# Optimization experiments

Measured on AMD Instinct MI355X. Metric: run time of the kernel, lower is better.

## Reference

```python
import jax, jax.numpy as jnp
import numpy as np

N = 4096          # residues (2 chains x 2048)
CHAINS = 2
LMAX = 2
L = (LMAX + 1) ** 2            # 9 spherical coefficients
BBC = 32                       # bb_channels
NBB = 3                        # n_bb_atoms - 1
SPH = BBC + NBB                # 35 sphere channels fed to attention
KNN = 20
LRK = 40
HEADS = 8
HC = 32
VC = HC // 4                   # attn_value_channels = 8
EDGE_F = 32                    # 16 RBF + 16 positional
L_IDX = np.repeat(np.arange(LMAX + 1), 2 * np.arange(LMAX + 1) + 1)  # degree of each of the 9 coeffs


def so3_linear(x, w, b):
    # x: [N,L,Cin]; w: [LMAX+1,Cin,Cout] shared across m within each degree l; bias only on l=0
    out = jnp.einsum('nlc,lcd->nld', x, w[L_IDX])
    return out.at[:, 0, :].add(b)


def _rbf(d):
    mu = jnp.linspace(0.0, 20.0, 16)
    sigma = 20.0 / 16
    return jnp.exp(-(((d[..., None] - mu) / sigma) ** 2))


def _edge_pos_embed(src, dst):
    d = (src - dst).astype(jnp.float32)
    freq = jnp.exp(jnp.arange(0, 16, 2, dtype=jnp.float32) * (-np.log(10000.0) / 16))
    ang = d[:, None] * freq
    return jnp.concatenate([jnp.cos(ang), jnp.sin(ang)], axis=-1)


def setup_inputs():
    key = jax.random.key(0)
    ks = jax.random.split(key, 16)
    n = lambda i, shp, s=1.0: jax.random.normal(ks[i], shp) * s
    return {
        'X_ca': n(0, (N, 3), 10.0),
        'bb_rel': n(1, (N, NBB, 3)),
        'bb_features': n(2, (N, L, BBC)),
        'batch': jnp.repeat(jnp.arange(CHAINS), N // CHAINS),
        'x_mask': jax.random.uniform(ks[3], (N,)) < 0.02,
        'noising_mask': jax.random.uniform(ks[4], (N,)) < 0.5,
        'attn_w1': n(5, (2 * SPH + EDGE_F, HC), 0.05), 'attn_b1': jnp.zeros((HC,)),
        'attn_w2': n(6, (HC, HEADS), 0.05), 'attn_b2': jnp.zeros((HEADS,)),
        'wv': n(7, (LMAX + 1, SPH, HEADS * VC), 0.05), 'bv': jnp.zeros((HEADS * VC,)),
        'wo': n(8, (LMAX + 1, HEADS * VC, BBC), 0.05), 'bo': jnp.zeros((BBC,)),
        'wg': n(9, (BBC, BBC), 0.05), 'bg': jnp.zeros((BBC,)),
        'wf': n(10, (LMAX + 1, BBC, BBC), 0.05), 'bf': jnp.zeros((BBC,)),
        'w_xca': n(11, (LMAX + 1, BBC, 1), 0.05), 'b_xca': jnp.zeros((1,)),
        'w_gate': n(12, (BBC, 1), 0.05), 'b_gate': jnp.zeros((1,)),
        'w_bb': n(13, (LMAX + 1, BBC, NBB), 0.05), 'b_bb': jnp.zeros((NBB,)),
    }


def reference(X_ca, bb_rel, bb_features, batch, x_mask, noising_mask,
              attn_w1, attn_b1, attn_w2, attn_b2, wv, bv, wo, bo, wg, bg, wf, bf,
              w_xca, b_xca, w_gate, b_gate, w_bb, b_bb):
    Nn = X_ca.shape[0]
    BIG = jnp.float32(1e30)
    # ---- graph construction (knn_graph + sample_inv_cubic_edges) ----
    x2 = jnp.sum(X_ca * X_ca, axis=-1)
    D2 = jnp.maximum(x2[:, None] + x2[None, :] - 2.0 * (X_ca @ X_ca.T), 0.0)  # [N,N]
    same = batch[:, None] == batch[None, :]
    eye = jnp.eye(Nn, dtype=bool)
    mask_pair = x_mask[:, None] | x_mask[None, :]
    invalid = (~same) | eye | mask_pair
    knn_idx = jax.lax.top_k(-jnp.where(invalid, BIG, D2), KNN)[1]   # [N,KNN] sources per target
    # long-range: inverse-cubic distance weights, Gumbel top-k sampling, excluding knn picks
    logits = jnp.where(invalid, -BIG, -1.5 * jnp.log(D2 + 1e-6))
    rows = jnp.arange(Nn)[:, None]
    logits = logits.at[rows, knn_idx].set(-BIG)
    gumb = jax.random.gumbel(jax.random.key(1), (Nn, Nn))
    lr_idx = jax.lax.top_k(logits + gumb, LRK)[1]                   # [N,LRK]
    src = jnp.concatenate([knn_idx.reshape(-1), lr_idx.reshape(-1)])
    dst = jnp.concatenate([jnp.repeat(jnp.arange(Nn), KNN), jnp.repeat(jnp.arange(Nn), LRK)])
    # ---- edge features: RBF(dist) + relative positional embedding ----
    dvec = X_ca[src] - X_ca[dst]
    dist = jnp.linalg.norm(dvec, axis=-1)
    edge_feat = jnp.concatenate([_rbf(dist), _edge_pos_embed(src, dst)], axis=-1)  # [M,32]
    # ---- assemble SO3 node embedding [N,L,35] ----
    node = jnp.zeros((Nn, L, SPH), X_ca.dtype)
    node = node.at[:, :, :BBC].set(bb_features)
    node = node.at[:, 1:4, BBC:].set(jnp.swapaxes(bb_rel, -1, -2))  # l=1 coeffs carry bb_rel
    node = node.at[:, 0, SPH - 1].set(noising_mask.astype(X_ca.dtype))
    # ---- equivariant graph attention (simplified TransBlockV2) ----
    inv = node[:, 0, :]                                             # invariant (l=0) features
    a_in = jnp.concatenate([inv[src], inv[dst], edge_feat], axis=-1)
    h = jax.nn.silu(a_in @ attn_w1 + attn_b1)
    logit = h @ attn_w2 + attn_b2                                   # [M,HEADS]
    mx = jax.ops.segment_max(logit, dst, num_segments=Nn)
    p = jnp.exp(logit - mx[dst])
    Z = jax.ops.segment_sum(p, dst, num_segments=Nn)
    alpha = p / (Z[dst] + 1e-9)                                     # segment softmax per target/head
    v = so3_linear(node, wv, bv)[src].reshape(-1, L, HEADS, VC)     # gather source values
    msg = (v * alpha[:, None, :, None]).reshape(-1, L, HEADS * VC)
    agg = jax.ops.segment_sum(msg, dst, num_segments=Nn)            # scatter to targets
    out = so3_linear(agg, wo, bo)                                   # [N,L,32]
    gate = jax.nn.silu(out[:, 0, :] @ wg + bg)                      # invariant-gated FFN
    out = out + so3_linear(out, wf, bf) * gate[:, None, :]
    # ---- coordinate / backbone updates ----
    upd_x = so3_linear(out, w_xca, b_xca)                           # [N,L,1]
    vec = upd_x[:, 1:4, 0]                                          # l=1 -> 3-vector
    g2 = jax.nn.softplus(out[:, 0, :] @ w_gate + b_gate)            # [N,1]
    new_X = X_ca + jnp.where(noising_mask[:, None], vec * g2, 0.0)
    upd_bb = so3_linear(out, w_bb, b_bb)                            # [N,L,3]
    dbb = jnp.swapaxes(upd_bb[:, 1:4, :], -1, -2)                   # [N,3,3]
    new_bb = bb_rel + jnp.where(noising_mask[:, None, None], dbb, 0.0)
    return new_X, new_bb, out
```

## Files before the change

kernel.cpp:

```cpp
#include <hip/hip_runtime.h>
#include <hip/hip_bf16.h>
#include <stdint.h>

#define NN 4096
#define CS 2048
#define KNN 20
#define LRK 40
#define EPN 60
#define NE (NN*EPN)
#define SPHC 35
#define BBCC 32
#define NHEAD 8
#define HVD 64
#define HCD 32
#define LT 9
#define MAXC 384

#define INVAL_D2 0xFFFFFFFEu
#define CONSUMED 0xFFFFFFFFu

__device__ __forceinline__ float bf2f(__hip_bfloat16 x) { return __bfloat162float(x); }

__device__ __forceinline__ float fast_exp(float x) {
  return __builtin_amdgcn_exp2f(x * 1.4426950408889634f);
}
__device__ __forceinline__ float fast_cos(float a) {
  float rev = a * 0.15915494309189535f;
  rev = rev - __builtin_rintf(rev);
  return __builtin_amdgcn_cosf(rev);
}
__device__ __forceinline__ float fast_sin(float a) {
  float rev = a * 0.15915494309189535f;
  rev = rev - __builtin_rintf(rev);
  return __builtin_amdgcn_sinf(rev);
}

__device__ __forceinline__ float neglogu_f(int i, int j) {
  uint32_t c = ((uint32_t)(i & 2047) << 12) | (uint32_t)j;
  const uint32_t ks0 = 0u, ks1 = 1u, ks2 = 0x1BD11BDBu;
  uint32_t x0 = c + ks0;
  uint32_t x1 = (c + 0x800000u) + ks1;
#define TF_R(r) { x0 += x1; x1 = (x1 << (r)) | (x1 >> (32 - (r))); x1 ^= x0; }
  TF_R(13) TF_R(15) TF_R(26) TF_R(6)   x0 += ks1; x1 += ks2 + 1u;
  TF_R(17) TF_R(29) TF_R(16) TF_R(24)  x0 += ks2; x1 += ks0 + 2u;
  TF_R(13) TF_R(15) TF_R(26) TF_R(6)   x0 += ks0; x1 += ks1 + 3u;
  TF_R(17) TF_R(29) TF_R(16) TF_R(24)  x0 += ks1; x1 += ks2 + 4u;
  TF_R(13) TF_R(15) TF_R(26) TF_R(6)   x0 += ks2; x1 += ks0 + 5u;
#undef TF_R
  uint32_t b = (i >= 2048) ? x1 : x0;
  float u = __uint_as_float((b >> 9) | 0x3F800000u) - 1.0f;
  u = u + 1.17549435e-38f;
  return -logf(u);
}

__global__ void prep_kernel(const float* __restrict__ X,
                            const int* __restrict__ batch,
                            const int* __restrict__ xmask,
                            float4* __restrict__ Xw, uint32_t* __restrict__ bm) {
#pragma clang fp contract(off)
  int n = blockIdx.x * blockDim.x + threadIdx.x;
  if (n >= NN) return;
  float x = X[n*3+0], y = X[n*3+1], z = X[n*3+2];
  float x2 = (x*x + y*y) + z*z;
  Xw[n] = make_float4(x, y, z, x2);
  bm[n] = ((uint32_t)batch[n] << 1) | (xmask[n] ? 1u : 0u);
}

__global__ __launch_bounds__(256) void nodeproj_kernel(const float* __restrict__ bbf,
                                                       const int* __restrict__ nmask,
                                                       const float* __restrict__ w1,
                                                       const float* __restrict__ b1,
                                                       float* __restrict__ Pn,
                                                       float* __restrict__ Pd) {
  int tid = threadIdx.x;
  int t = tid & 31;
  int n = blockIdx.x * 8 + (tid >> 5);
  float bv_ = bbf[(size_t)n * (LT*BBCC) + t];
  float an = 0.f, ad = b1[t];
  #pragma unroll 8
  for (int c = 0; c < BBCC; c++) {
    float bc = __shfl(bv_, (tid & 32) + c, 64);
    an = fmaf(bc, w1[c * HCD + t], an);
    ad = fmaf(bc, w1[(SPHC + c) * HCD + t], ad);
  }
  float nm = nmask[n] ? 1.f : 0.f;
  an = fmaf(nm, w1[34 * HCD + t], an);
  ad = fmaf(nm, w1[69 * HCD + t], ad);
  Pn[n * HCD + t] = an;
  Pd[n * HCD + t] = ad;
}

__device__ __forceinline__ void sel2l(uint32_t* val, uint32_t* hist2,
                                      uint32_t* candk, uint32_t* candp,
                                      uint32_t* sh, int* sel,
                                      int k, int base, int cb, int tid) {
  {
    uint4* h4 = (uint4*)hist2;
    uint4 z; z.x = 0; z.y = 0; z.z = 0; z.w = 0;
    h4[tid] = z; h4[tid + 256] = z;
  }
  if (tid == 0) { sh[2] = 0; sh[3] = 0; }
  __syncthreads();
  #pragma unroll
  for (int q = 0; q < 8; q++) {
    uint32_t key = val[tid + (q << 8)];
    atomicAdd(&hist2[key >> 21], 1u);
  }
  __syncthreads();
  uint32_t h[8], s = 0;
  #pragma unroll
  for (int q = 0; q < 8; q++) { h[q] = hist2[tid*8 + q]; s += h[q]; }
  uint32_t cum = s;
  #pragma unroll
  for (int off = 1; off < 64; off <<= 1) {
    uint32_t o = __shfl_up(cum, off, 64);
    if ((tid & 63) >= off) cum += o;
  }
  if ((tid & 63) == 63) sh[8 + (tid >> 6)] = cum;
  __syncthreads();
  uint32_t woff = 0;
  for (int w = 0; w < (tid >> 6); w++) woff += sh[8 + w];
  uint32_t cumAll = cum + woff;
  uint32_t cumBefore = cumAll - s;
  uint32_t rk = (uint32_t)k;
  if (rk > cumBefore && rk <= cumAll) {
    uint32_t rloc = rk - cumBefore, lp = 0;
    bool done = false;
    #pragma unroll
    for (int q = 0; q < 8; q++) {
      lp += h[q];
      if (!done && rloc <= lp) { sh[0] = (uint32_t)(tid*8 + q); sh[1] = rloc - (lp - h[q]); done = true; }
    }
  }
  __syncthreads();
  const uint32_t B = sh[0], r = sh[1];
  #pragma unroll
  for (int q = 0; q < 8; q++) {
    int pos = tid + (q << 8);
    uint32_t key = val[pos];
    if ((key >> 21) == B) {
      uint32_t idx = atomicAdd(&sh[2], 1u);
      if (idx < MAXC) { candk[idx] = key; candp[idx] = (uint32_t)pos; }
    }
  }
  __syncthreads();
  int m = (int)sh[2]; if (m > MAXC) m = MAXC;
  if (tid < 64) {
    for (int ci = tid; ci < m; ci += 64) {
      unsigned long long k64 = ((unsigned long long)candk[ci] << 32) | candp[ci];
      uint32_t rank = 0;
      for (int j = 0; j < m; j++) {
        unsigned long long o = ((unsigned long long)candk[j] << 32) | candp[j];
        rank += (o < k64) ? 1u : 0u;
      }
      if (rank == r - 1) { sh[0] = candk[ci]; sh[1] = candp[ci]; }
    }
  }
  __syncthreads();
  const uint32_t vstar = sh[0], istar = sh[1];
  #pragma unroll
  for (int q = 0; q < 8; q++) {
    int pos = tid + (q << 8);
    uint32_t key = val[pos];
    if (key < vstar || (key == vstar && (uint32_t)pos <= istar)) {
      uint32_t slot = atomicAdd(&sh[3], 1u);
      sel[base + (int)slot] = cb + pos;
    }
  }
  __syncthreads();
}

__global__ __launch_bounds__(256) void select_kernel(const float4* __restrict__ Xw,
                                                     const uint32_t* __restrict__ bm,
                                                     int* __restrict__ srcO) {
#pragma clang fp contract(off)
  __shared__ uint32_t val[CS];
  __shared__ uint32_t hist2[2048];
  __shared__ uint32_t candk[MAXC];
  __shared__ uint32_t candp[MAXC];
  __shared__ uint32_t sh[12];
  __shared__ int sel[EPN];
  const int i = blockIdx.x, tid = threadIdx.x;
  const uint32_t bmi = bm[i];

  if (bmi & 1u) {
    if (tid < KNN) srcO[(size_t)i * EPN + tid] = tid;
    else if (tid < EPN) srcO[(size_t)i * EPN + tid] = tid - KNN;
    return;
  }
  const int cb = (int)(bmi >> 1) * CS;
  const float4 xi = Xw[i];

  #pragma unroll
  for (int q = 0; q < 8; q++) {
    int pos = tid + (q << 8);
    int j = cb + pos;
    float4 xj = Xw[j];
    uint32_t bmj = bm[j];
    bool inval = ((bmj & 1u) != 0u) || (j == i);
    float dot = xi.x*xj.x + xi.y*xj.y + xi.z*xj.z;
    float d2r = (xi.w + xj.w) - 2.0f*dot;
    float d2 = d2r > 0.0f ? d2r : 0.0f;
    val[pos] = inval ? INVAL_D2 : __float_as_uint(d2);
  }
  __syncthreads();

  sel2l(val, hist2, candk, candp, sh, sel, KNN, 0, cb, tid);

  if (tid < KNN) val[sel[tid] - cb] = CONSUMED;
  __syncthreads();

  #pragma unroll
  for (int q = 0; q < 8; q++) {
    int pos = tid + (q << 8);
    uint32_t v = val[pos];
    uint32_t skey;
    if (v >= INVAL_D2) skey = CONSUMED;
    else {
      float d2p = __uint_as_float(v) + 1e-6f;
      float w = d2p * sqrtf(d2p) * neglogu_f(i, cb + pos);
      skey = __float_as_uint(w);
    }
    val[pos] = skey;
  }
  __syncthreads();

  sel2l(val, hist2, candk, candp, sh, sel, LRK, KNN, cb, tid);

  if (tid < EPN) srcO[(size_t)i * EPN + tid] = sel[tid];
}

__global__ __launch_bounds__(256) void vmat_kernel(const float* __restrict__ bbf,
                                                   const float* __restrict__ bbrel,
                                                   const int* __restrict__ nmask,
                                                   const float* __restrict__ wv,
                                                   const float* __restrict__ bv,
                                                   __hip_bfloat16* __restrict__ V) {
  int row = blockIdx.x * 4 + (threadIdx.x >> 6);
  int d = threadIdx.x & 63;
  if (row >= NN * LT) return;
  int n = row / LT, l = row % LT;
  int li = (l == 0) ? 0 : (l < 4 ? 1 : 2);
  const float* w = wv + (size_t)li * SPHC * HVD;
  float acc = (l == 0) ? bv[d] : 0.f;
  const float* nb = bbf + (size_t)(n*LT + l) * BBCC;
  for (int c = 0; c < BBCC; c++) acc = fmaf(nb[c], w[c*HVD + d], acc);
  if (l >= 1 && l < 4) {
    for (int b = 0; b < 3; b++)
      acc = fmaf(bbrel[(size_t)(n*3 + b)*3 + (l-1)], w[(32+b)*HVD + d], acc);
  }
  if (l == 0) acc = fmaf(nmask[n] ? 1.f : 0.f, w[34*HVD + d], acc);
  V[(size_t)row * HVD + d] = __float2bfloat16(acc);
}

__global__ __launch_bounds__(256) void edge_kernel(const int* __restrict__ src,
                                                   const float4* __restrict__ Xw,
                                                   const float* __restrict__ Pn,
                                                   const float* __restrict__ Pd,
                                                   const float* __restrict__ w1,
                                                   const float* __restrict__ w2,
                                                   const float* __restrict__ b2,
                                                   float* __restrict__ logitO) {
  const float FR[8] = {1.0f, 0.31622776601683794f, 0.1f, 0.031622776601683794f,
                       0.01f, 0.0031622776601683794f, 0.001f, 0.00031622776601683794f};
  __shared__ float w1cf[BBCC][HCD];
  __shared__ float w2f[HCD][NHEAD];
  __shared__ float b2f[NHEAD];
  __shared__ float ef[8][BBCC];
  __shared__ float hbuf[8][HCD];
  int tid = threadIdx.x;
  for (int q = tid; q < BBCC*HCD; q += 256) w1cf[q >> 5][q & 31] = w1[70*HCD + q];
  if (tid < HCD*NHEAD) w2f[tid >> 3][tid & 7] = w2[tid];
  if (tid < NHEAD) b2f[tid] = b2[tid];
  int sub = tid >> 5, t = tid & 31;
  int e = blockIdx.x * 8 + sub;
  int d = e / EPN;
  int s = src[e];
  float4 xs = Xw[s], xd = Xw[d];
  float dx = xs.x - xd.x, dy = xs.y - xd.y, dz = xs.z - xd.z;
  float dist = sqrtf(dx*dx + dy*dy + dz*dz);
  if (t < 16) {
    float mu = (20.0f / 15.0f) * (float)t;
    float zz = (dist - mu) / 1.25f;
    ef[sub][t] = fast_exp(-zz * zz);
  } else {
    int k = t - 16;
    float del = (float)(s - d);
    float a = del * FR[k & 7];
    ef[sub][t] = (k < 8) ? fast_cos(a) : fast_sin(a);
  }
  __syncthreads();
  float a = Pn[s * HCD + t] + Pd[d * HCD + t];
  #pragma unroll
  for (int k = 0; k < BBCC; k++) a = fmaf(ef[sub][k], w1cf[k][t], a);
  hbuf[sub][t] = a / (1.f + fast_exp(-a));
  __syncthreads();
  if (tid < 64) {
    int e2 = tid >> 3, hh = tid & 7;
    float lg = b2f[hh];
    #pragma unroll
    for (int c = 0; c < HCD; c++) lg = fmaf(hbuf[e2][c], w2f[c][hh], lg);
    logitO[(size_t)(blockIdx.x * 8 + e2) * NHEAD + hh] = lg;
  }
}

__global__ __launch_bounds__(256) void node_kernel(const int* __restrict__ src,
                                                  const float* __restrict__ logit,
                                                  const __hip_bfloat16* __restrict__ V,
                                                  const float* __restrict__ wo,
                                                  const float* __restrict__ bo,
                                                  const float* __restrict__ wg,
                                                  const float* __restrict__ bg,
                                                  const float* __restrict__ wf,
                                                  const float* __restrict__ bfb,
                                                  const float* __restrict__ w_xca,
                                                  const float* __restrict__ w_gate,
                                                  const float* __restrict__ b_gate,
                                                  const float* __restrict__ w_bb,
                                                  const float* __restrict__ X,
                                                  const float* __restrict__ bbrel,
                                                  const int* __restrict__ nmask,
                                                  float* __restrict__ out) {
  const int n = blockIdx.x, t = threadIdx.x;
  __shared__ float alpha[EPN][NHEAD];
  __shared__ int slist[EPN];
  __shared__ float aggp[4][LT][HVD];
  __shared__ float agg[LT][HVD];
  __shared__ float o0[LT][BBCC];
  __shared__ float ofin[LT][BBCC];
  __shared__ float gate[BBCC];
  if (t < EPN) slist[t] = src[(size_t)n * EPN + t];
  for (int idx = t; idx < EPN * NHEAD; idx += 256)
    alpha[idx >> 3][idx & 7] = logit[(size_t)n * 480 + idx];
  __syncthreads();
  if (t < NHEAD) {
    float m = -1e30f;
    for (int e = 0; e < EPN; e++) m = fmaxf(m, alpha[e][t]);
    float Z = 0.f;
    for (int e = 0; e < EPN; e++) { float p = expf(alpha[e][t] - m); alpha[e][t] = p; Z += p; }
    float iz = 1.f / (Z + 1e-9f);
    for (int e = 0; e < EPN; e++) alpha[e][t] *= iz;
  }
  __syncthreads();
  {
    const int wave = t >> 6, lane = t & 63;
    const int h = lane >> 3;
    float acc[LT];
    #pragma unroll
    for (int l = 0; l < LT; l++) acc[l] = 0.f;
    const int e0 = wave * 15;
    for (int e = e0; e < e0 + 15; e++) {
      const __hip_bfloat16* Vp = V + (size_t)slist[e] * (LT * HVD) + lane;
      float a = alpha[e][h];
      #pragma unroll
      for (int l = 0; l < LT; l++) acc[l] = fmaf(a, bf2f(Vp[l * HVD]), acc[l]);
    }
    #pragma unroll
    for (int l = 0; l < LT; l++) aggp[wave][l][lane] = acc[l];
  }
  __syncthreads();
  for (int idx = t; idx < LT * HVD; idx += 256) {
    int l = idx >> 6, c = idx & 63;
    agg[l][c] = (aggp[0][l][c] + aggp[1][l][c]) + (aggp[2][l][c] + aggp[3][l][c]);
  }
  __syncthreads();
  for (int idx = t; idx < LT * BBCC; idx += 256) {
    int l = idx >> 5, d = idx & 31;
    int li = (l == 0) ? 0 : (l < 4 ? 1 : 2);
    float a = (l == 0) ? bo[d] : 0.f;
    const float* w = wo + (size_t)li * HVD * BBCC;
    for (int c = 0; c < HVD; c++) a = fmaf(agg[l][c], w[c * BBCC + d], a);
    o0[l][d] = a;
  }
  __syncthreads();
  if (t < BBCC) {
    float a = bg[t];
    for (int c = 0; c < BBCC; c++) a = fmaf(o0[0][c], wg[c * BBCC + t], a);
    gate[t] = a / (1.f + expf(-a));
  }
  __syncthreads();
  for (int idx = t; idx < LT * BBCC; idx += 256) {
    int l = idx >> 5, d = idx & 31;
    int li = (l == 0) ? 0 : (l < 4 ? 1 : 2);
    float a = (l == 0) ? bfb[d] : 0.f;
    const float* w = wf + (size_t)li * BBCC * BBCC;
    for (int c = 0; c < BBCC; c++) a = fmaf(o0[l][c], w[c * BBCC + d], a);
    float r = o0[l][d] + a * gate[d];
    ofin[l][d] = r;
    out[49152 + (size_t)n * 288 + idx] = r;
  }
  __syncthreads();
  if (t < 16) {
    float a2 = b_gate[0];
    for (int c = 0; c < BBCC; c++) a2 = fmaf(ofin[0][c], w_gate[c], a2);
    float g2 = fmaxf(a2, 0.f) + log1pf(expf(-fabsf(a2)));
    bool noise = nmask[n] != 0;
    if (t < 3) {
      float a = 0.f;
      for (int d2 = 0; d2 < BBCC; d2++) a = fmaf(ofin[1 + t][d2], w_xca[32 + d2], a);
      float nx = X[n * 3 + t] + (noise ? a * g2 : 0.f);
      out[(size_t)n * 3 + t] = nx;
    }
    if (t < 9) {
      int b = t / 3, c = t % 3;
      float a = 0.f;
      for (int d2 = 0; d2 < BBCC; d2++) a = fmaf(ofin[1 + c][d2], w_bb[(32 + d2) * 3 + b], a);
      float nb = bbrel[(size_t)(n * 3 + b) * 3 + c] + (noise ? a : 0.f);
      out[12288 + (size_t)n * 9 + b * 3 + c] = nb;
    }
  }
}

extern "C" void kernel_launch(void* const* d_in, const int* in_sizes, int n_in,
                              void* d_out, int out_size, void* d_ws, size_t ws_size,
                              hipStream_t stream) {
  (void)in_sizes; (void)n_in; (void)out_size;
  const float* X      = (const float*)d_in[0];
  const float* bbrel  = (const float*)d_in[1];
  const float* bbf    = (const float*)d_in[2];
  const int* batch    = (const int*)d_in[3];
  const int* xmask    = (const int*)d_in[4];
  const int* nmask    = (const int*)d_in[5];
  const float* w1     = (const float*)d_in[6];
  const float* b1     = (const float*)d_in[7];
  const float* w2     = (const float*)d_in[8];
  const float* b2     = (const float*)d_in[9];
  const float* wv     = (const float*)d_in[10];
  const float* bv     = (const float*)d_in[11];
  const float* wo     = (const float*)d_in[12];
  const float* bo     = (const float*)d_in[13];
  const float* wg     = (const float*)d_in[14];
  const float* bg     = (const float*)d_in[15];
  const float* wf     = (const float*)d_in[16];
  const float* bfb    = (const float*)d_in[17];
  const float* w_xca  = (const float*)d_in[18];
  const float* w_gate = (const float*)d_in[20];
  const float* b_gate = (const float*)d_in[21];
  const float* w_bb   = (const float*)d_in[22];

  if (ws_size < 18939904) return;
  char* ws = (char*)d_ws;
  uint32_t* bmp   = (uint32_t*)(ws + 0);
  int*      srcl  = (int*)(ws + 16384);
  float*    logit = (float*)(ws + 999424);
  __hip_bfloat16* V = (__hip_bfloat16*)(ws + 8863744);
  float*    Pn    = (float*)(ws + 8863744);
  float*    Pd    = (float*)(ws + 9388032);
  float4*   Xw    = (float4*)(ws + 9912320);
  float*    out   = (float*)d_out;

  prep_kernel<<<NN / 256, 256, 0, stream>>>(X, batch, xmask, Xw, bmp);
  nodeproj_kernel<<<NN / 8, 256, 0, stream>>>(bbf, nmask, w1, b1, Pn, Pd);
  select_kernel<<<NN, 256, 0, stream>>>(Xw, bmp, srcl);
  edge_kernel<<<NE / 8, 256, 0, stream>>>(srcl, Xw, Pn, Pd, w1, w2, b2, logit);
  vmat_kernel<<<(NN * LT) / 4, 256, 0, stream>>>(bbf, bbrel, nmask, wv, bv, V);
  node_kernel<<<NN, 256, 0, stream>>>(srcl, logit, V, wo, bo, wg, bg, wf, bfb,
                                      w_xca, w_gate, b_gate, w_bb, X, bbrel, nmask, out);
}
```

Baseline: 286.3 us.

## Merge small kernels into shared launches and vectorize V gather in node kernel

Combines prep and node projection into one launch, and folds the V-matrix projection into the select kernel's grid as extra blocks, so independent work shares launches and can overlap. The node kernel's value aggregation now loads each source row with 16-byte vector loads and unpacks bf16 pairs with bit shifts, in place of scalar strided bf16 loads. Pn/Pd/Xw are moved in the workspace so they no longer alias V, which is now written concurrently. Risks include the shared-memory footprint of select applying to the vmat blocks, and the tail-row handling in the vectorized gather.

```diff
diff --git a/kernel.cpp b/kernel.cpp
--- a/kernel.cpp
+++ b/kernel.cpp
@@ -15,11 +15,15 @@
 #define HCD 32
 #define LT 9
 #define MAXC 384
+#define VMB ((NN*LT)/4)
+#define NPB (NN/8)
 
 #define INVAL_D2 0xFFFFFFFEu
 #define CONSUMED 0xFFFFFFFFu
 
 __device__ __forceinline__ float bf2f(__hip_bfloat16 x) { return __bfloat162float(x); }
+__device__ __forceinline__ float bflo(uint32_t d) { return __uint_as_float(d << 16); }
+__device__ __forceinline__ float bfhi(uint32_t d) { return __uint_as_float(d & 0xFFFF0000u); }
 
 __device__ __forceinline__ float fast_exp(float x) {
   return __builtin_amdgcn_exp2f(x * 1.4426950408889634f);
@@ -53,41 +57,43 @@
   return -logf(u);
 }
 
-__global__ void prep_kernel(const float* __restrict__ X,
-                            const int* __restrict__ batch,
-                            const int* __restrict__ xmask,
-                            float4* __restrict__ Xw, uint32_t* __restrict__ bm) {
+__global__ __launch_bounds__(256) void prep_proj_kernel(const float* __restrict__ X,
+                                                        const int* __restrict__ batch,
+                                                        const int* __restrict__ xmask,
+                                                        const int* __restrict__ nmask,
+                                                        const float* __restrict__ bbf,
+                                                        const float* __restrict__ w1,
+                                                        const float* __restrict__ b1,
+                                                        float4* __restrict__ Xw,
+                                                        uint32_t* __restrict__ bm,
+                                                        float* __restrict__ Pn,
+                                                        float* __restrict__ Pd) {
 #pragma clang fp contract(off)
-  int n = blockIdx.x * blockDim.x + threadIdx.x;
-  if (n >= NN) return;
-  float x = X[n*3+0], y = X[n*3+1], z = X[n*3+2];
-  float x2 = (x*x + y*y) + z*z;
-  Xw[n] = make_float4(x, y, z, x2);
-  bm[n] = ((uint32_t)batch[n] << 1) | (xmask[n] ? 1u : 0u);
-}
-
-__global__ __launch_bounds__(256) void nodeproj_kernel(const float* __restrict__ bbf,
-                                                       const int* __restrict__ nmask,
-                                                       const float* __restrict__ w1,
-                                                       const float* __restrict__ b1,
-                                                       float* __restrict__ Pn,
-                                                       float* __restrict__ Pd) {
   int tid = threadIdx.x;
-  int t = tid & 31;
-  int n = blockIdx.x * 8 + (tid >> 5);
-  float bv_ = bbf[(size_t)n * (LT*BBCC) + t];
-  float an = 0.f, ad = b1[t];
-  #pragma unroll 8
-  for (int c = 0; c < BBCC; c++) {
-    float bc = __shfl(bv_, (tid & 32) + c, 64);
-    an = fmaf(bc, w1[c * HCD + t], an);
-    ad = fmaf(bc, w1[(SPHC + c) * HCD + t], ad);
-  }
-  float nm = nmask[n] ? 1.f : 0.f;
-  an = fmaf(nm, w1[34 * HCD + t], an);
-  ad = fmaf(nm, w1[69 * HCD + t], ad);
-  Pn[n * HCD + t] = an;
-  Pd[n * HCD + t] = ad;
+  if (blockIdx.x < NPB) {
+    int t = tid & 31;
+    int n = blockIdx.x * 8 + (tid >> 5);
+    float bv_ = bbf[(size_t)n * (LT*BBCC) + t];
+    float an = 0.f, ad = b1[t];
+    #pragma unroll 8
+    for (int c = 0; c < BBCC; c++) {
+      float bc = __shfl(bv_, (tid & 32) + c, 64);
+      an = fmaf(bc, w1[c * HCD + t], an);
+      ad = fmaf(bc, w1[(SPHC + c) * HCD + t], ad);
+    }
+    float nm = nmask[n] ? 1.f : 0.f;
+    an = fmaf(nm, w1[34 * HCD + t], an);
+    ad = fmaf(nm, w1[69 * HCD + t], ad);
+    Pn[n * HCD + t] = an;
+    Pd[n * HCD + t] = ad;
+  } else {
+    int n = (blockIdx.x - NPB) * 256 + tid;
+    if (n >= NN) return;
+    float x = X[n*3+0], y = X[n*3+1], z = X[n*3+2];
+    float x2 = (x*x + y*y) + z*z;
+    Xw[n] = make_float4(x, y, z, x2);
+    bm[n] = ((uint32_t)batch[n] << 1) | (xmask[n] ? 1u : 0u);
+  }
 }
 
 __device__ __forceinline__ void sel2l(uint32_t* val, uint32_t* hist2,
@@ -170,17 +176,42 @@
   __syncthreads();
 }
 
-__global__ __launch_bounds__(256) void select_kernel(const float4* __restrict__ Xw,
-                                                     const uint32_t* __restrict__ bm,
-                                                     int* __restrict__ srcO) {
+__global__ __launch_bounds__(256) void select_vmat_kernel(const float4* __restrict__ Xw,
+                                                          const uint32_t* __restrict__ bm,
+                                                          int* __restrict__ srcO,
+                                                          const float* __restrict__ bbf,
+                                                          const float* __restrict__ bbrel,
+                                                          const int* __restrict__ nmask,
+                                                          const float* __restrict__ wv,
+                                                          const float* __restrict__ bv,
+                                                          __hip_bfloat16* __restrict__ V) {
 #pragma clang fp contract(off)
+  const int tid = threadIdx.x;
+  if (blockIdx.x >= NN) {
+    int row = (blockIdx.x - NN) * 4 + (tid >> 6);
+    int d = tid & 63;
+    if (row >= NN * LT) return;
+    int n = row / LT, l = row % LT;
+    int li = (l == 0) ? 0 : (l < 4 ? 1 : 2);
+    const float* w = wv + (size_t)li * SPHC * HVD;
+    float acc = (l == 0) ? bv[d] : 0.f;
+    const float* nb = bbf + (size_t)(n*LT + l) * BBCC;
+    for (int c = 0; c < BBCC; c++) acc = fmaf(nb[c], w[c*HVD + d], acc);
+    if (l >= 1 && l < 4) {
+      for (int b = 0; b < 3; b++)
+        acc = fmaf(bbrel[(size_t)(n*3 + b)*3 + (l-1)], w[(32+b)*HVD + d], acc);
+    }
+    if (l == 0) acc = fmaf(nmask[n] ? 1.f : 0.f, w[34*HVD + d], acc);
+    V[(size_t)row * HVD + d] = __float2bfloat16(acc);
+    return;
+  }
   __shared__ uint32_t val[CS];
   __shared__ uint32_t hist2[2048];
   __shared__ uint32_t candk[MAXC];
   __shared__ uint32_t candp[MAXC];
   __shared__ uint32_t sh[12];
   __shared__ int sel[EPN];
-  const int i = blockIdx.x, tid = threadIdx.x;
+  const int i = blockIdx.x;
   const uint32_t bmi = bm[i];
 
   if (bmi & 1u) {
@@ -228,29 +259,6 @@
   sel2l(val, hist2, candk, candp, sh, sel, LRK, KNN, cb, tid);
 
   if (tid < EPN) srcO[(size_t)i * EPN + tid] = sel[tid];
-}
-
-__global__ __launch_bounds__(256) void vmat_kernel(const float* __restrict__ bbf,
-                                                   const float* __restrict__ bbrel,
-                                                   const int* __restrict__ nmask,
-                                                   const float* __restrict__ wv,
-                                                   const float* __restrict__ bv,
-                                                   __hip_bfloat16* __restrict__ V) {
-  int row = blockIdx.x * 4 + (threadIdx.x >> 6);
-  int d = threadIdx.x & 63;
-  if (row >= NN * LT) return;
-  int n = row / LT, l = row % LT;
-  int li = (l == 0) ? 0 : (l < 4 ? 1 : 2);
-  const float* w = wv + (size_t)li * SPHC * HVD;
-  float acc = (l == 0) ? bv[d] : 0.f;
-  const float* nb = bbf + (size_t)(n*LT + l) * BBCC;
-  for (int c = 0; c < BBCC; c++) acc = fmaf(nb[c], w[c*HVD + d], acc);
-  if (l >= 1 && l < 4) {
-    for (int b = 0; b < 3; b++)
-      acc = fmaf(bbrel[(size_t)(n*3 + b)*3 + (l-1)], w[(32+b)*HVD + d], acc);
-  }
-  if (l == 0) acc = fmaf(nmask[n] ? 1.f : 0.f, w[34*HVD + d], acc);
-  V[(size_t)row * HVD + d] = __float2bfloat16(acc);
 }
 
 __global__ __launch_bounds__(256) void edge_kernel(const int* __restrict__ src,
@@ -344,19 +352,38 @@
   __syncthreads();
   {
     const int wave = t >> 6, lane = t & 63;
-    const int h = lane >> 3;
-    float acc[LT];
+    const int hM = lane & 7;
+    const int hT = (lane & 31) >> 2;
+    float accm[8];
     #pragma unroll
-    for (int l = 0; l < LT; l++) acc[l] = 0.f;
+    for (int j = 0; j < 8; j++) accm[j] = 0.f;
+    float acct0 = 0.f, acct1 = 0.f;
     const int e0 = wave * 15;
+    #pragma unroll 5
     for (int e = e0; e < e0 + 15; e++) {
-      const __hip_bfloat16* Vp = V + (size_t)slist[e] * (LT * HVD) + lane;
-      float a = alpha[e][h];
-      #pragma unroll
-      for (int l = 0; l < LT; l++) acc[l] = fmaf(a, bf2f(Vp[l * HVD]), acc[l]);
-    }
+      const uint32_t* Vr = (const uint32_t*)(V + (size_t)slist[e] * (LT * HVD));
+      uint4 m = ((const uint4*)Vr)[lane];
+      uint32_t tl = (lane < 32) ? Vr[256 + lane] : 0u;
+      float am = alpha[e][hM];
+      float at = alpha[e][hT];
+      accm[0] = fmaf(am, bflo(m.x), accm[0]);
+      accm[1] = fmaf(am, bfhi(m.x), accm[1]);
+      accm[2] = fmaf(am, bflo(m.y), accm[2]);
+      accm[3] = fmaf(am, bfhi(m.y), accm[3]);
+      accm[4] = fmaf(am, bflo(m.z), accm[4]);
+      accm[5] = fmaf(am, bfhi(m.z), accm[5]);
+      accm[6] = fmaf(am, bflo(m.w), accm[6]);
+      accm[7] = fmaf(am, bfhi(m.w), accm[7]);
+      acct0 = fmaf(at, bflo(tl), acct0);
+      acct1 = fmaf(at, bfhi(tl), acct1);
+    }
+    const int l = lane >> 3, c0 = (lane & 7) * 8;
     #pragma unroll
-    for (int l = 0; l < LT; l++) aggp[wave][l][lane] = acc[l];
+    for (int j = 0; j < 8; j++) aggp[wave][l][c0 + j] = accm[j];
+    if (lane < 32) {
+      aggp[wave][8][2*lane]     = acct0;
+      aggp[wave][8][2*lane + 1] = acct1;
+    }
   }
   __syncthreads();
   for (int idx = t; idx < LT * HVD; idx += 256) {
@@ -444,16 +471,16 @@
   int*      srcl  = (int*)(ws + 16384);
   float*    logit = (float*)(ws + 999424);
   __hip_bfloat16* V = (__hip_bfloat16*)(ws + 8863744);
-  float*    Pn    = (float*)(ws + 8863744);
-  float*    Pd    = (float*)(ws + 9388032);
-  float4*   Xw    = (float4*)(ws + 9912320);
+  float*    Pn    = (float*)(ws + 13582336);
+  float*    Pd    = (float*)(ws + 14106624);
+  float4*   Xw    = (float4*)(ws + 14630912);
   float*    out   = (float*)d_out;
 
-  prep_kernel<<<NN / 256, 256, 0, stream>>>(X, batch, xmask, Xw, bmp);
-  nodeproj_kernel<<<NN / 8, 256, 0, stream>>>(bbf, nmask, w1, b1, Pn, Pd);
-  select_kernel<<<NN, 256, 0, stream>>>(Xw, bmp, srcl);
+  prep_proj_kernel<<<NPB + 16, 256, 0, stream>>>(X, batch, xmask, nmask, bbf, w1, b1,
+                                                 Xw, bmp, Pn, Pd);
+  select_vmat_kernel<<<NN + VMB, 256, 0, stream>>>(Xw, bmp, srcl, bbf, bbrel, nmask,
+                                                   wv, bv, V);
   edge_kernel<<<NE / 8, 256, 0, stream>>>(srcl, Xw, Pn, Pd, w1, w2, b2, logit);
-  vmat_kernel<<<(NN * LT) / 4, 256, 0, stream>>>(bbf, bbrel, nmask, wv, bv, V);
   node_kernel<<<NN, 256, 0, stream>>>(srcl, logit, V, wo, bo, wg, bg, wf, bfb,
                                       w_xca, w_gate, b_gate, w_bb, X, bbrel, nmask, out);
 }
```

Measured after the change: 273.3 us. 4.5% less time.
